# Performance work log

Measured on AMD Instinct MI355X. Metric: run time of the kernel, lower is better.

Reference implementation:

```python
import jax, jax.numpy as jnp
import numpy as np

N_NODES = 50000
N_EDGES = 800000
IN_CH = 128
HID = 128
OUT_CH = 64
BN_EPS = 1e-5


def setup_inputs() -> dict:
    key = jax.random.key(0)
    ks = jax.random.split(key, 12)
    glorot = lambda k, fi, fo: jax.random.normal(k, (fi, fo), jnp.float32) * np.sqrt(2.0 / (fi + fo))
    return {
        "x": jax.random.normal(ks[0], (N_NODES, IN_CH), jnp.float32),
        "edge_index": jax.random.randint(ks[1], (2, N_EDGES), 0, N_NODES, jnp.int64),
        "W1": glorot(ks[2], IN_CH, HID), "b1": jnp.zeros((HID,), jnp.float32),
        "gamma1": jnp.ones((HID,), jnp.float32), "beta1": jnp.zeros((HID,), jnp.float32),
        "W2": glorot(ks[3], HID, HID), "b2": jnp.zeros((HID,), jnp.float32),
        "gamma2": jnp.ones((HID,), jnp.float32), "beta2": jnp.zeros((HID,), jnp.float32),
        "Wmu": glorot(ks[4], HID, OUT_CH), "bmu": jnp.zeros((OUT_CH,), jnp.float32),
        "Wls": glorot(ks[5], HID, OUT_CH), "bls": jnp.zeros((OUT_CH,), jnp.float32),
    }


def _gcn(h, W, b, src, dst, norm, n):
    # GCNConv: linear transform, then normalized scatter-add aggregation
    h = h @ W                                    # [N, out]
    msg = h[src] * norm[:, None]                 # [E+N, out] gathered messages
    out = jax.ops.segment_sum(msg, dst, num_segments=n)
    return out + b


def _batch_norm(h, gamma, beta):
    mu = jnp.mean(h, axis=0)
    var = jnp.mean(jnp.square(h - mu), axis=0)   # biased var (BatchNorm1d train mode)
    return (h - mu) * jax.lax.rsqrt(var + BN_EPS) * gamma + beta


def reference(x, edge_index, W1, b1, gamma1, beta1, W2, b2, gamma2, beta2, Wmu, bmu, Wls, bls):
    n = x.shape[0]
    loops = jnp.arange(n, dtype=edge_index.dtype)
    src = jnp.concatenate([edge_index[0], loops])  # add self-loops
    dst = jnp.concatenate([edge_index[1], loops])
    # symmetric normalization deg^-1/2 A_hat deg^-1/2 (same for every layer)
    deg = jax.ops.segment_sum(jnp.ones_like(src, jnp.float32), dst, num_segments=n)
    dinv = jax.lax.rsqrt(deg)                     # deg >= 1 because of self-loops
    norm = dinv[src] * dinv[dst]

    h = jax.nn.relu(_batch_norm(_gcn(x, W1, b1, src, dst, norm, n), gamma1, beta1))
    h = jax.nn.relu(_batch_norm(_gcn(h, W2, b2, src, dst, norm, n), gamma2, beta2))
    mu = _gcn(h, Wmu, bmu, src, dst, norm, n)
    logstd = _gcn(h, Wls, bls, src, dst, norm, n)
    return (mu, logstd)
```

## Files before the change

### kernel.cpp

```cpp
#include <hip/hip_runtime.h>

#define NN 50000
#define NE 800000
#define C 128
#define OUTC 64
#define BN_EPS 1e-5f
#define INVN (1.0f / 50000.0f)
#define NBLK 49

__device__ __forceinline__ unsigned short f2bf(float f) {
    unsigned u = __float_as_uint(f);
    u += 0x7fffu + ((u >> 16) & 1u);
    return (unsigned short)(u >> 16);
}


__global__ __launch_bounds__(256) void hist_kernel(const int* __restrict__ dstp, int* __restrict__ cnt) {
    int e = blockIdx.x * 256 + threadIdx.x;
    if (e < NE) atomicAdd(&cnt[dstp[e]], 1);
}

__global__ __launch_bounds__(256) void scan1_kernel(const int* __restrict__ cnt, int* __restrict__ rowptr,
                                                    float* __restrict__ dinv, int* __restrict__ bsum) {
    __shared__ int lds[256];
    int tid = threadIdx.x;
    int base = blockIdx.x * 1024 + tid * 4;
    int v[4];
    int s = 0;
    #pragma unroll
    for (int j = 0; j < 4; ++j) { int i = base + j; v[j] = (i < NN) ? cnt[i] : 0; s += v[j]; }
    lds[tid] = s;
    __syncthreads();
    for (int off = 1; off < 256; off <<= 1) {
        int x = (tid >= off) ? lds[tid - off] : 0;
        __syncthreads();
        lds[tid] += x;
        __syncthreads();
    }
    int excl = lds[tid] - s;
    #pragma unroll
    for (int j = 0; j < 4; ++j) {
        int i = base + j;
        if (i < NN) {
            rowptr[i] = excl;
            dinv[i] = rsqrtf((float)(v[j] + 1));
        }
        excl += v[j];
    }
    if (tid == 255) bsum[blockIdx.x] = lds[255];
}

__global__ __launch_bounds__(256) void scan3_kernel(const int* __restrict__ bsum, int* __restrict__ rowptr,
                                                    int* __restrict__ wpos) {
    __shared__ int boff;
    int tid = threadIdx.x;
    if (tid < 64) {
        int orig = (tid < NBLK) ? bsum[tid] : 0;
        int v = orig;
        #pragma unroll
        for (int off = 1; off < 64; off <<= 1) {
            int x = __shfl_up(v, off);
            if (tid >= off) v += x;
        }
        if (tid == (int)blockIdx.x) boff = v - orig;
    }
    __syncthreads();
    int off = boff;
    int base = blockIdx.x * 1024 + tid * 4;
    #pragma unroll
    for (int j = 0; j < 4; ++j) {
        int i = base + j;
        if (i < NN) { int r = rowptr[i] + off; rowptr[i] = r; wpos[i] = r; }
    }
    if (blockIdx.x == 0 && tid == 0) rowptr[NN] = NE;
}

__global__ __launch_bounds__(256) void fill_kernel(const int* __restrict__ srcp, const int* __restrict__ dstp,
                                                   int* __restrict__ wpos, int* __restrict__ col) {
    int e = blockIdx.x * 256 + threadIdx.x;
    if (e < NE) {
        int d = dstp[e];
        int p = atomicAdd(&wpos[d], 1);
        col[p] = srcp[e];
    }
}


template<bool TRANS, bool SPLITW>
__global__ __launch_bounds__(256) void gemm_kernel(
    const float* __restrict__ A, const float* __restrict__ W, const float* __restrict__ Wb,
    const float* __restrict__ sums, const float* __restrict__ gamma, const float* __restrict__ beta,
    const float* __restrict__ dinv, unsigned short* __restrict__ out)
{
    __shared__ float Ws[64][128];
    __shared__ float xT[128][36];
    int tid = threadIdx.x;
    int row0 = blockIdx.x * 32;

    #pragma unroll
    for (int i = 0; i < 4; ++i) {
        int idx = tid + i * 256;
        int r = idx >> 5;
        int k4 = (idx & 31) * 4;
        int gr = row0 + r;
        float vv[4] = {0.f, 0.f, 0.f, 0.f};
        if (gr < NN) {
            float4 v = *(const float4*)&A[(size_t)gr * C + k4];
            vv[0] = v.x; vv[1] = v.y; vv[2] = v.z; vv[3] = v.w;
        }
        if (TRANS) {
            #pragma unroll
            for (int j = 0; j < 4; ++j) {
                int k = k4 + j;
                float mean = sums[k] * INVN;
                float var = fmaf(-mean, mean, sums[128 + k] * INVN);
                float sc = gamma[k] * rsqrtf(var + BN_EPS);
                float sh = fmaf(-mean, sc, beta[k]);
                vv[j] = fmaxf(fmaf(vv[j], sc, sh), 0.f);
            }
        }
        xT[k4 + 0][r] = vv[0]; xT[k4 + 1][r] = vv[1]; xT[k4 + 2][r] = vv[2]; xT[k4 + 3][r] = vv[3];
    }

    float acc[4][4] = {};
    int cg = (tid & 31) * 4;
    int rg = (tid >> 5) * 4;

    for (int kh = 0; kh < 2; ++kh) {
        __syncthreads();
        #pragma unroll
        for (int i = 0; i < 8; ++i) {
            int fi = tid + i * 256;
            int k = fi >> 5;
            int c4 = (fi & 31) * 4;
            float4 wv;
            if (!SPLITW) wv = *(const float4*)&W[(size_t)(kh * 64 + k) * C + c4];
            else         wv = (c4 < 64) ? *(const float4*)&W[(size_t)(kh * 64 + k) * 64 + c4]
                                        : *(const float4*)&Wb[(size_t)(kh * 64 + k) * 64 + (c4 - 64)];
            *(float4*)&Ws[k][c4] = wv;
        }
        __syncthreads();
        #pragma unroll 8
        for (int k = 0; k < 64; ++k) {
            float4 a = *(const float4*)&xT[kh * 64 + k][rg];
            float4 b = *(const float4*)&Ws[k][cg];
            acc[0][0] = fmaf(a.x, b.x, acc[0][0]); acc[0][1] = fmaf(a.x, b.y, acc[0][1]);
            acc[0][2] = fmaf(a.x, b.z, acc[0][2]); acc[0][3] = fmaf(a.x, b.w, acc[0][3]);
            acc[1][0] = fmaf(a.y, b.x, acc[1][0]); acc[1][1] = fmaf(a.y, b.y, acc[1][1]);
            acc[1][2] = fmaf(a.y, b.z, acc[1][2]); acc[1][3] = fmaf(a.y, b.w, acc[1][3]);
            acc[2][0] = fmaf(a.z, b.x, acc[2][0]); acc[2][1] = fmaf(a.z, b.y, acc[2][1]);
            acc[2][2] = fmaf(a.z, b.z, acc[2][2]); acc[2][3] = fmaf(a.z, b.w, acc[2][3]);
            acc[3][0] = fmaf(a.w, b.x, acc[3][0]); acc[3][1] = fmaf(a.w, b.y, acc[3][1]);
            acc[3][2] = fmaf(a.w, b.z, acc[3][2]); acc[3][3] = fmaf(a.w, b.w, acc[3][3]);
        }
    }

    #pragma unroll
    for (int i = 0; i < 4; ++i) {
        int row = row0 + rg + i;
        if (row < NN) {
            float rs = dinv[row];
            ushort4 o;
            o.x = f2bf(acc[i][0] * rs); o.y = f2bf(acc[i][1] * rs);
            o.z = f2bf(acc[i][2] * rs); o.w = f2bf(acc[i][3] * rs);
            *(ushort4*)&out[(size_t)row * C + cg] = o;
        }
    }
}


template<bool SPLIT>
__global__ __launch_bounds__(256) void agg_kernel(
    const unsigned short* __restrict__ t, const int* __restrict__ rowptr, const int* __restrict__ col,
    const float* __restrict__ dinv, const float* __restrict__ bmu, const float* __restrict__ bls,
    float* __restrict__ outb, float* __restrict__ out2)
{
    int wave = threadIdx.x >> 6;
    int lane = threadIdx.x & 63;
    int row = blockIdx.x * 4 + wave;
    int c = lane * 2;
    const unsigned short* tp = t + c;
    float di = dinv[row];
    int e0 = rowptr[row], e1 = rowptr[row + 1];

    unsigned vs = *(const unsigned*)&tp[(size_t)row * C];
    float a0 = __uint_as_float(vs << 16);
    float a1 = __uint_as_float(vs & 0xffff0000u);

    int e = e0;
    for (; e + 3 < e1; e += 4) {
        int s0 = col[e], s1 = col[e + 1], s2 = col[e + 2], s3 = col[e + 3];
        unsigned v0 = *(const unsigned*)&tp[(size_t)s0 * C];
        unsigned v1 = *(const unsigned*)&tp[(size_t)s1 * C];
        unsigned v2 = *(const unsigned*)&tp[(size_t)s2 * C];
        unsigned v3 = *(const unsigned*)&tp[(size_t)s3 * C];
        a0 += (__uint_as_float(v0 << 16) + __uint_as_float(v1 << 16))
            + (__uint_as_float(v2 << 16) + __uint_as_float(v3 << 16));
        a1 += (__uint_as_float(v0 & 0xffff0000u) + __uint_as_float(v1 & 0xffff0000u))
            + (__uint_as_float(v2 & 0xffff0000u) + __uint_as_float(v3 & 0xffff0000u));
    }
    for (; e < e1; ++e) {
        int s = col[e];
        unsigned v = *(const unsigned*)&tp[(size_t)s * C];
        a0 += __uint_as_float(v << 16);
        a1 += __uint_as_float(v & 0xffff0000u);
    }

    if (!SPLIT) {
        *(float2*)&outb[(size_t)row * C + c] = make_float2(di * a0, di * a1);
    } else {
        if (c < 64) *(float2*)&outb[(size_t)row * OUTC + c]
                        = make_float2(fmaf(di, a0, bmu[c]), fmaf(di, a1, bmu[c + 1]));
        else        *(float2*)&out2[(size_t)row * OUTC + (c - 64)]
                        = make_float2(fmaf(di, a0, bls[c - 64]), fmaf(di, a1, bls[c - 63]));
    }
}


__global__ __launch_bounds__(256) void bnstats_kernel(const float* __restrict__ h, float* __restrict__ sums) {
    int c = threadIdx.x & 127;
    int hh = threadIdx.x >> 7;
    float s = 0.f, sq = 0.f;
    for (int r = blockIdx.x * 2 + hh; r < NN; r += gridDim.x * 2) {
        float v = h[(size_t)r * C + c];
        s += v; sq = fmaf(v, v, sq);
    }
    __shared__ float ls[256], lq[256];
    ls[threadIdx.x] = s; lq[threadIdx.x] = sq;
    __syncthreads();
    if (hh == 0) {
        atomicAdd(&sums[c], s + ls[c + 128]);
        atomicAdd(&sums[128 + c], sq + lq[c + 128]);
    }
}


extern "C" void kernel_launch(void* const* d_in, const int* in_sizes, int n_in,
                              void* d_out, int out_size, void* d_ws, size_t ws_size,
                              hipStream_t stream) {
    (void)in_sizes; (void)n_in; (void)out_size; (void)ws_size;
    const float* x      = (const float*)d_in[0];
    const int*   ei     = (const int*)d_in[1];
    const float* W1     = (const float*)d_in[2];
    const float* gamma1 = (const float*)d_in[4];
    const float* beta1  = (const float*)d_in[5];
    const float* W2     = (const float*)d_in[6];
    const float* gamma2 = (const float*)d_in[8];
    const float* beta2  = (const float*)d_in[9];
    const float* Wmu    = (const float*)d_in[10];
    const float* bmu    = (const float*)d_in[11];
    const float* Wls    = (const float*)d_in[12];
    const float* bls    = (const float*)d_in[13];

    float* outmu = (float*)d_out;
    float* outls = outmu + (size_t)NN * OUTC;

    char* w = (char*)d_ws;
    size_t off = 0;
    auto alloc = [&](size_t bytes) { char* p = w + off; off = (off + bytes + 255) & ~(size_t)255; return p; };
    unsigned short* t = (unsigned short*)alloc(sizeof(unsigned short) * NN * C);
    float* aggb   = (float*)alloc(sizeof(float) * NN * C);
    int*   cnt    = (int*)  alloc(sizeof(int) * NN);
    float* sums   = (float*)alloc(sizeof(float) * 512);
    int*   rowptr = (int*)  alloc(sizeof(int) * (NN + 1));
    int*   wpos   = (int*)  alloc(sizeof(int) * NN);
    int*   col    = (int*)  alloc(sizeof(int) * NE);
    float* dinv   = (float*)alloc(sizeof(float) * NN);
    int*   bsum   = (int*)  alloc(sizeof(int) * 64);
    float* sumsA = sums; float* sumsB = sums + 256;

    const int* srcp = ei;
    const int* dstp = ei + NE;

    size_t zspan = (size_t)((char*)(sums + 512) - (char*)cnt);
    hipMemsetAsync(cnt, 0, zspan, stream);

    hist_kernel<<<(NE + 255) / 256, 256, 0, stream>>>(dstp, cnt);
    scan1_kernel<<<NBLK, 256, 0, stream>>>(cnt, rowptr, dinv, bsum);
    scan3_kernel<<<NBLK, 256, 0, stream>>>(bsum, rowptr, wpos);
    fill_kernel<<<(NE + 255) / 256, 256, 0, stream>>>(srcp, dstp, wpos, col);

    const int GB = (NN + 31) / 32;
    const int AB = NN / 4;

    gemm_kernel<false, false><<<GB, 256, 0, stream>>>(x, W1, nullptr, nullptr, nullptr, nullptr, dinv, t);
    agg_kernel<false><<<AB, 256, 0, stream>>>(t, rowptr, col, dinv, nullptr, nullptr, aggb, nullptr);
    bnstats_kernel<<<400, 256, 0, stream>>>(aggb, sumsA);

    gemm_kernel<true, false><<<GB, 256, 0, stream>>>(aggb, W2, nullptr, sumsA, gamma1, beta1, dinv, t);
    agg_kernel<false><<<AB, 256, 0, stream>>>(t, rowptr, col, dinv, nullptr, nullptr, aggb, nullptr);
    bnstats_kernel<<<400, 256, 0, stream>>>(aggb, sumsB);

    gemm_kernel<true, true><<<GB, 256, 0, stream>>>(aggb, Wmu, Wls, sumsB, gamma2, beta2, dinv, t);
    agg_kernel<true><<<AB, 256, 0, stream>>>(t, rowptr, col, dinv, bmu, bls, outmu, outls);
}
```

Before: 448.4 us.

## Use bf16 MFMA for GEMMs and widen aggregation gathers to 16-byte loads

Replaces the FP32 LDS-tiled GEMM with bf16 MFMA 16x16x32 instructions. Weights are prepacked once into the fragment layout by a new prep kernel, and activations are converted to bf16 in registers. The aggregation kernel is restructured so each wave handles four edges at a time, with 16 lanes each loading 8 bf16 values (16 bytes) and a final cross-lane shuffle reduction. This cuts GEMM ALU work and gather instruction count, in exchange for rounding GEMM inputs to bf16 and extra masking and shuffle overhead.

After: 408.1 us. -9.0%, faster.

```diff
diff --git a/kernel.cpp b/kernel.cpp
--- a/kernel.cpp
+++ b/kernel.cpp
@@ -8,10 +8,17 @@
 #define INVN (1.0f / 50000.0f)
 #define NBLK 49
 
+typedef __attribute__((ext_vector_type(8))) short bf16x8;
+typedef __attribute__((ext_vector_type(4))) float f32x4;
+typedef __attribute__((ext_vector_type(8))) unsigned short u16x8;
+
 __device__ __forceinline__ unsigned short f2bf(float f) {
     unsigned u = __float_as_uint(f);
     u += 0x7fffu + ((u >> 16) & 1u);
     return (unsigned short)(u >> 16);
+}
+__device__ __forceinline__ float bf2f(unsigned short s) {
+    return __uint_as_float((unsigned)s << 16);
 }
 
 
@@ -86,84 +93,85 @@
 }
 
 
-template<bool TRANS, bool SPLITW>
+__global__ __launch_bounds__(256) void prep_kernel(const float* __restrict__ W1, const float* __restrict__ W2,
+                                                   const float* __restrict__ Wmu, const float* __restrict__ Wls,
+                                                   unsigned short* __restrict__ Wpk) {
+    int idx = blockIdx.x * 256 + threadIdx.x;
+    if (idx >= 3 * 2048) return;
+    int which = idx >> 11;
+    int r = idx & 2047;
+    int l = r & 63;
+    int nt = (r >> 6) & 7;
+    int kt = r >> 9;
+    int m = l & 15, kg = l >> 4;
+    int c = nt * 16 + m;
+    bf16x8 o;
+    #pragma unroll
+    for (int j = 0; j < 8; ++j) {
+        int k = kt * 32 + kg * 8 + j;
+        float w;
+        if (which == 0)      w = W1[k * 128 + c];
+        else if (which == 1) w = W2[k * 128 + c];
+        else                 w = (c < 64) ? Wmu[k * 64 + c] : Wls[k * 64 + (c - 64)];
+        o[j] = (short)f2bf(w);
+    }
+    *(bf16x8*)&Wpk[(size_t)which * 16384 + (size_t)r * 8] = o;
+}
+
+
+template<bool TRANS>
 __global__ __launch_bounds__(256) void gemm_kernel(
-    const float* __restrict__ A, const float* __restrict__ W, const float* __restrict__ Wb,
+    const float* __restrict__ A, const unsigned short* __restrict__ Wpk,
     const float* __restrict__ sums, const float* __restrict__ gamma, const float* __restrict__ beta,
     const float* __restrict__ dinv, unsigned short* __restrict__ out)
 {
-    __shared__ float Ws[64][128];
-    __shared__ float xT[128][36];
     int tid = threadIdx.x;
-    int row0 = blockIdx.x * 32;
-
-    #pragma unroll
-    for (int i = 0; i < 4; ++i) {
-        int idx = tid + i * 256;
-        int r = idx >> 5;
-        int k4 = (idx & 31) * 4;
-        int gr = row0 + r;
-        float vv[4] = {0.f, 0.f, 0.f, 0.f};
-        if (gr < NN) {
-            float4 v = *(const float4*)&A[(size_t)gr * C + k4];
-            vv[0] = v.x; vv[1] = v.y; vv[2] = v.z; vv[3] = v.w;
-        }
+    int wv = tid >> 6, l = tid & 63;
+    int m = l & 15, kg = l >> 4;
+    int rhalf = wv & 1, chalf = wv >> 1;
+    int row = blockIdx.x * 32 + rhalf * 16 + m;
+    int rowc = min(row, NN - 1);
+    const float* Ar = A + (size_t)rowc * C;
+
+    f32x4 acc[4] = {};
+
+    #pragma unroll
+    for (int kt = 0; kt < 4; ++kt) {
+        int k0 = kt * 32 + kg * 8;
+        float4 x0 = *(const float4*)&Ar[k0];
+        float4 x1 = *(const float4*)&Ar[k0 + 4];
+        float av[8] = {x0.x, x0.y, x0.z, x0.w, x1.x, x1.y, x1.z, x1.w};
         if (TRANS) {
             #pragma unroll
-            for (int j = 0; j < 4; ++j) {
-                int k = k4 + j;
+            for (int j = 0; j < 8; ++j) {
+                int k = k0 + j;
                 float mean = sums[k] * INVN;
                 float var = fmaf(-mean, mean, sums[128 + k] * INVN);
                 float sc = gamma[k] * rsqrtf(var + BN_EPS);
                 float sh = fmaf(-mean, sc, beta[k]);
-                vv[j] = fmaxf(fmaf(vv[j], sc, sh), 0.f);
+                av[j] = fmaxf(fmaf(av[j], sc, sh), 0.f);
             }
         }
-        xT[k4 + 0][r] = vv[0]; xT[k4 + 1][r] = vv[1]; xT[k4 + 2][r] = vv[2]; xT[k4 + 3][r] = vv[3];
-    }
-
-    float acc[4][4] = {};
-    int cg = (tid & 31) * 4;
-    int rg = (tid >> 5) * 4;
-
-    for (int kh = 0; kh < 2; ++kh) {
-        __syncthreads();
-        #pragma unroll
-        for (int i = 0; i < 8; ++i) {
-            int fi = tid + i * 256;
-            int k = fi >> 5;
-            int c4 = (fi & 31) * 4;
-            float4 wv;
-            if (!SPLITW) wv = *(const float4*)&W[(size_t)(kh * 64 + k) * C + c4];
-            else         wv = (c4 < 64) ? *(const float4*)&W[(size_t)(kh * 64 + k) * 64 + c4]
-                                        : *(const float4*)&Wb[(size_t)(kh * 64 + k) * 64 + (c4 - 64)];
-            *(float4*)&Ws[k][c4] = wv;
-        }
-        __syncthreads();
-        #pragma unroll 8
-        for (int k = 0; k < 64; ++k) {
-            float4 a = *(const float4*)&xT[kh * 64 + k][rg];
-            float4 b = *(const float4*)&Ws[k][cg];
-            acc[0][0] = fmaf(a.x, b.x, acc[0][0]); acc[0][1] = fmaf(a.x, b.y, acc[0][1]);
-            acc[0][2] = fmaf(a.x, b.z, acc[0][2]); acc[0][3] = fmaf(a.x, b.w, acc[0][3]);
-            acc[1][0] = fmaf(a.y, b.x, acc[1][0]); acc[1][1] = fmaf(a.y, b.y, acc[1][1]);
-            acc[1][2] = fmaf(a.y, b.z, acc[1][2]); acc[1][3] = fmaf(a.y, b.w, acc[1][3]);
-            acc[2][0] = fmaf(a.z, b.x, acc[2][0]); acc[2][1] = fmaf(a.z, b.y, acc[2][1]);
-            acc[2][2] = fmaf(a.z, b.z, acc[2][2]); acc[2][3] = fmaf(a.z, b.w, acc[2][3]);
-            acc[3][0] = fmaf(a.w, b.x, acc[3][0]); acc[3][1] = fmaf(a.w, b.y, acc[3][1]);
-            acc[3][2] = fmaf(a.w, b.z, acc[3][2]); acc[3][3] = fmaf(a.w, b.w, acc[3][3]);
-        }
-    }
-
-    #pragma unroll
-    for (int i = 0; i < 4; ++i) {
-        int row = row0 + rg + i;
-        if (row < NN) {
-            float rs = dinv[row];
-            ushort4 o;
-            o.x = f2bf(acc[i][0] * rs); o.y = f2bf(acc[i][1] * rs);
-            o.z = f2bf(acc[i][2] * rs); o.w = f2bf(acc[i][3] * rs);
-            *(ushort4*)&out[(size_t)row * C + cg] = o;
+        bf16x8 af;
+        #pragma unroll
+        for (int j = 0; j < 8; ++j) af[j] = (short)f2bf(av[j]);
+        #pragma unroll
+        for (int n = 0; n < 4; ++n) {
+            int nt = chalf * 4 + n;
+            bf16x8 bfr = *(const bf16x8*)&Wpk[(size_t)((kt * 8 + nt) * 64 + l) * 8];
+            acc[n] = __builtin_amdgcn_mfma_f32_16x16x32_bf16(af, bfr, acc[n], 0, 0, 0);
+        }
+    }
+
+    int ro = blockIdx.x * 32 + rhalf * 16 + kg * 4;
+    #pragma unroll
+    for (int r = 0; r < 4; ++r) {
+        int orow = ro + r;
+        if (orow < NN) {
+            float di = dinv[orow];
+            #pragma unroll
+            for (int n = 0; n < 4; ++n)
+                out[(size_t)orow * C + (chalf * 4 + n) * 16 + m] = f2bf(di * acc[n][r]);
         }
     }
 }
@@ -175,44 +183,75 @@
     const float* __restrict__ dinv, const float* __restrict__ bmu, const float* __restrict__ bls,
     float* __restrict__ outb, float* __restrict__ out2)
 {
-    int wave = threadIdx.x >> 6;
-    int lane = threadIdx.x & 63;
+    int wave = threadIdx.x >> 6, lane = threadIdx.x & 63;
     int row = blockIdx.x * 4 + wave;
-    int c = lane * 2;
-    const unsigned short* tp = t + c;
-    float di = dinv[row];
+    int q = lane & 15, eg = lane >> 4;
+    const unsigned short* tq = t + q * 8;
     int e0 = rowptr[row], e1 = rowptr[row + 1];
-
-    unsigned vs = *(const unsigned*)&tp[(size_t)row * C];
-    float a0 = __uint_as_float(vs << 16);
-    float a1 = __uint_as_float(vs & 0xffff0000u);
-
-    int e = e0;
-    for (; e + 3 < e1; e += 4) {
-        int s0 = col[e], s1 = col[e + 1], s2 = col[e + 2], s3 = col[e + 3];
-        unsigned v0 = *(const unsigned*)&tp[(size_t)s0 * C];
-        unsigned v1 = *(const unsigned*)&tp[(size_t)s1 * C];
-        unsigned v2 = *(const unsigned*)&tp[(size_t)s2 * C];
-        unsigned v3 = *(const unsigned*)&tp[(size_t)s3 * C];
-        a0 += (__uint_as_float(v0 << 16) + __uint_as_float(v1 << 16))
-            + (__uint_as_float(v2 << 16) + __uint_as_float(v3 << 16));
-        a1 += (__uint_as_float(v0 & 0xffff0000u) + __uint_as_float(v1 & 0xffff0000u))
-            + (__uint_as_float(v2 & 0xffff0000u) + __uint_as_float(v3 & 0xffff0000u));
-    }
-    for (; e < e1; ++e) {
-        int s = col[e];
-        unsigned v = *(const unsigned*)&tp[(size_t)s * C];
-        a0 += __uint_as_float(v << 16);
-        a1 += __uint_as_float(v & 0xffff0000u);
-    }
-
-    if (!SPLIT) {
-        *(float2*)&outb[(size_t)row * C + c] = make_float2(di * a0, di * a1);
-    } else {
-        if (c < 64) *(float2*)&outb[(size_t)row * OUTC + c]
-                        = make_float2(fmaf(di, a0, bmu[c]), fmaf(di, a1, bmu[c + 1]));
-        else        *(float2*)&out2[(size_t)row * OUTC + (c - 64)]
-                        = make_float2(fmaf(di, a0, bls[c - 64]), fmaf(di, a1, bls[c - 63]));
+    float a[8] = {};
+
+    for (int e = e0; e < e1; e += 16) {
+        int lim = e1 - 1;
+        u16x8 v[4];
+        float msk[4];
+        #pragma unroll
+        for (int b = 0; b < 4; ++b) {
+            int i = e + b * 4 + eg;
+            msk[b] = (i < e1) ? 1.f : 0.f;
+            if (e + b * 4 < e1) {
+                int s = col[min(i, lim)];
+                v[b] = *(const u16x8*)&tq[(size_t)s * C];
+            } else {
+                v[b] = (u16x8)0;
+                msk[b] = 0.f;
+            }
+        }
+        #pragma unroll
+        for (int b = 0; b < 4; ++b) {
+            #pragma unroll
+            for (int j = 0; j < 8; ++j)
+                a[j] = fmaf(msk[b], bf2f(v[b][j]), a[j]);
+        }
+    }
+
+    {
+        u16x8 vs = *(const u16x8*)&tq[(size_t)row * C];
+        float ms = (eg == 0) ? 1.f : 0.f;
+        #pragma unroll
+        for (int j = 0; j < 8; ++j)
+            a[j] = fmaf(ms, bf2f(vs[j]), a[j]);
+    }
+
+    #pragma unroll
+    for (int j = 0; j < 8; ++j) {
+        a[j] += __shfl_xor(a[j], 16);
+        a[j] += __shfl_xor(a[j], 32);
+    }
+
+    if (eg == 0) {
+        float di = dinv[row];
+        int c = q * 8;
+        if (!SPLIT) {
+            *(float4*)&outb[(size_t)row * C + c]     = make_float4(di*a[0], di*a[1], di*a[2], di*a[3]);
+            *(float4*)&outb[(size_t)row * C + c + 4] = make_float4(di*a[4], di*a[5], di*a[6], di*a[7]);
+        } else {
+            if (c < 64) {
+                float4 b0 = *(const float4*)&bmu[c];
+                float4 b1 = *(const float4*)&bmu[c + 4];
+                *(float4*)&outb[(size_t)row * OUTC + c]
+                    = make_float4(fmaf(di,a[0],b0.x), fmaf(di,a[1],b0.y), fmaf(di,a[2],b0.z), fmaf(di,a[3],b0.w));
+                *(float4*)&outb[(size_t)row * OUTC + c + 4]
+                    = make_float4(fmaf(di,a[4],b1.x), fmaf(di,a[5],b1.y), fmaf(di,a[6],b1.z), fmaf(di,a[7],b1.w));
+            } else {
+                int cc = c - 64;
+                float4 b0 = *(const float4*)&bls[cc];
+                float4 b1 = *(const float4*)&bls[cc + 4];
+                *(float4*)&out2[(size_t)row * OUTC + cc]
+                    = make_float4(fmaf(di,a[0],b0.x), fmaf(di,a[1],b0.y), fmaf(di,a[2],b0.z), fmaf(di,a[3],b0.w));
+                *(float4*)&out2[(size_t)row * OUTC + cc + 4]
+                    = make_float4(fmaf(di,a[4],b1.x), fmaf(di,a[5],b1.y), fmaf(di,a[6],b1.z), fmaf(di,a[7],b1.w));
+            }
+        }
     }
 }
 
@@ -267,6 +306,7 @@
     int*   col    = (int*)  alloc(sizeof(int) * NE);
     float* dinv   = (float*)alloc(sizeof(float) * NN);
     int*   bsum   = (int*)  alloc(sizeof(int) * 64);
+    unsigned short* Wpk = (unsigned short*)alloc(sizeof(unsigned short) * 3 * 16384);
     float* sumsA = sums; float* sumsB = sums + 256;
 
     const int* srcp = ei;
@@ -279,18 +319,19 @@
     scan1_kernel<<<NBLK, 256, 0, stream>>>(cnt, rowptr, dinv, bsum);
     scan3_kernel<<<NBLK, 256, 0, stream>>>(bsum, rowptr, wpos);
     fill_kernel<<<(NE + 255) / 256, 256, 0, stream>>>(srcp, dstp, wpos, col);
+    prep_kernel<<<24, 256, 0, stream>>>(W1, W2, Wmu, Wls, Wpk);
 
     const int GB = (NN + 31) / 32;
     const int AB = NN / 4;
 
-    gemm_kernel<false, false><<<GB, 256, 0, stream>>>(x, W1, nullptr, nullptr, nullptr, nullptr, dinv, t);
+    gemm_kernel<false><<<GB, 256, 0, stream>>>(x, Wpk, nullptr, nullptr, nullptr, dinv, t);
     agg_kernel<false><<<AB, 256, 0, stream>>>(t, rowptr, col, dinv, nullptr, nullptr, aggb, nullptr);
     bnstats_kernel<<<400, 256, 0, stream>>>(aggb, sumsA);
 
-    gemm_kernel<true, false><<<GB, 256, 0, stream>>>(aggb, W2, nullptr, sumsA, gamma1, beta1, dinv, t);
+    gemm_kernel<true><<<GB, 256, 0, stream>>>(aggb, Wpk + 16384, sumsA, gamma1, beta1, dinv, t);
     agg_kernel<false><<<AB, 256, 0, stream>>>(t, rowptr, col, dinv, nullptr, nullptr, aggb, nullptr);
     bnstats_kernel<<<400, 256, 0, stream>>>(aggb, sumsB);
 
-    gemm_kernel<true, true><<<GB, 256, 0, stream>>>(aggb, Wmu, Wls, sumsB, gamma2, beta2, dinv, t);
+    gemm_kernel<true><<<GB, 256, 0, stream>>>(aggb, Wpk + 32768, sumsB, gamma2, beta2, dinv, t);
     agg_kernel<true><<<AB, 256, 0, stream>>>(t, rowptr, col, dinv, bmu, bls, outmu, outls);
 }
```
